# Kernel optimization log

Hardware: AMD Instinct MI355X
Metric: run time of the kernel (lower is better)

The kernel has to match this reference:

```python
import jax, jax.numpy as jnp
import numpy as np

N, IN, HID, OUT = 18432, 1024, 4096, 4096


def _quantize_per_channel(w):
    # symmetric per-output-channel int8 quantization: scale = max|w|/127
    scale = jnp.max(jnp.abs(w), axis=1) / 127.0  # [rows]
    scale = jnp.maximum(scale, 1e-8)
    w_int8 = jnp.clip(jnp.round(w / scale[:, None]), -127, 127).astype(jnp.int8)
    return w_int8, scale.astype(jnp.float32)


def setup_inputs() -> dict:
    key = jax.random.key(0)
    kx, k1, kb1, k2, kb2 = jax.random.split(key, 5)
    x = jax.random.normal(kx, (N, IN), dtype=jnp.float32)
    # kaiming-uniform-ish float weights, then per-channel int8 quantize
    bound1 = 1.0 / np.sqrt(IN)
    bound2 = 1.0 / np.sqrt(HID)
    w1 = jax.random.uniform(k1, (HID, IN), minval=-bound1, maxval=bound1, dtype=jnp.float32)
    w2 = jax.random.uniform(k2, (OUT, HID), minval=-bound2, maxval=bound2, dtype=jnp.float32)
    w1_int8, w1_scale = _quantize_per_channel(w1)
    w2_int8, w2_scale = _quantize_per_channel(w2)
    b1 = jax.random.uniform(kb1, (HID,), minval=-bound1, maxval=bound1, dtype=jnp.float32)
    b2 = jax.random.uniform(kb2, (OUT,), minval=-bound2, maxval=bound2, dtype=jnp.float32)
    return {"x": x, "w1_int8": w1_int8, "w1_scale": w1_scale, "b1": b1,
            "w2_int8": w2_int8, "w2_scale": w2_scale, "b2": b2}


def reference(x, w1_int8, w1_scale, b1, w2_int8, w2_scale, b2):
    # W8A16 dequant GEMM + fused GELU (layer 1)
    w1 = w1_int8.astype(jnp.float32) * w1_scale[:, None]  # [HID, IN]
    h = jax.nn.gelu(x @ w1.T + b1, approximate=False)      # [N, HID]
    # W8A16 dequant GEMM (layer 2)
    w2 = w2_int8.astype(jnp.float32) * w2_scale[:, None]  # [OUT, HID]
    return h @ w2.T + b2                                   # [N, OUT]
```

## Files before the change

### kernel.cpp

```cpp
#include <hip/hip_runtime.h>
#include <math.h>

#define NROWS 18432
#define IN_DIM 1024
#define HID_DIM 4096
#define OUT_DIM 4096
#define NTN 16

typedef __attribute__((ext_vector_type(8))) short bf16x8;
typedef __attribute__((ext_vector_type(4))) float f32x4;

typedef const __attribute__((address_space(1))) char gchar;
typedef __attribute__((address_space(3))) char lchar;

__device__ __forceinline__ unsigned short f2bf(float f) {
    union { float f; unsigned u; } v; v.f = f;
    unsigned r = v.u + 0x7fffu + ((v.u >> 16) & 1u);
    return (unsigned short)(r >> 16);
}

__device__ __forceinline__ f32x4 MFMA16(bf16x8 a, bf16x8 b, f32x4 c) {
    return __builtin_amdgcn_mfma_f32_16x16x32_bf16(a, b, c, 0, 0, 0);
}


__global__ void cvt_f32_bf16_k(const float4* __restrict__ in, uint4* __restrict__ out, int nvec) {
    int i = blockIdx.x * blockDim.x + threadIdx.x;
    if (i >= nvec) return;
    float4 a = in[2 * i], b = in[2 * i + 1];
    union { unsigned short s[8]; uint4 v; } o;
    o.s[0] = f2bf(a.x); o.s[1] = f2bf(a.y); o.s[2] = f2bf(a.z); o.s[3] = f2bf(a.w);
    o.s[4] = f2bf(b.x); o.s[5] = f2bf(b.y); o.s[6] = f2bf(b.z); o.s[7] = f2bf(b.w);
    out[i] = o.v;
}

__global__ void cvt_i32_bf16_k(const int4* __restrict__ in, uint4* __restrict__ out, int nvec) {
    int i = blockIdx.x * blockDim.x + threadIdx.x;
    if (i >= nvec) return;
    int4 a = in[2 * i], b = in[2 * i + 1];
    union { unsigned short s[8]; uint4 v; } o;
    o.s[0] = f2bf((float)a.x); o.s[1] = f2bf((float)a.y);
    o.s[2] = f2bf((float)a.z); o.s[3] = f2bf((float)a.w);
    o.s[4] = f2bf((float)b.x); o.s[5] = f2bf((float)b.y);
    o.s[6] = f2bf((float)b.z); o.s[7] = f2bf((float)b.w);
    out[i] = o.v;
}

template<int EPI>
__global__ __launch_bounds__(512, 2)
void gemm3b(const unsigned short* __restrict__ A, const unsigned short* __restrict__ B,
            const float* __restrict__ scale, const float* __restrict__ bias,
            void* __restrict__ Cout, int K) {
    extern __shared__ __align__(16) char sm[];

    const int tid  = threadIdx.x;
    const int lane = tid & 63;
    const int wid  = tid >> 6;
    const int wm   = wid >> 2, wn = wid & 3;

    const int nwg  = gridDim.x;
    const int q    = nwg >> 3, r = nwg & 7;
    const int xcd  = blockIdx.x & 7, bidx = blockIdx.x >> 3;
    const int swz  = xcd * q + (xcd < r ? xcd : r) + bidx;
    const int tm   = swz / NTN, tn = swz % NTN;

    const size_t rowbytes = (size_t)K * 2;
    const char* Ag = (const char*)A + (size_t)tm * 256 * rowbytes;
    const char* Bg = (const char*)B + (size_t)tn * 256 * rowbytes;

    const int l16 = lane & 15;
    const int cg  = (lane >> 4) << 4;

    f32x4  acc[8][4] = {};
    bf16x8 af[4], ah[4], bl[2], bh[2];

    const int NT = K >> 5;

#define STAGE(GB, LB, UNIT, KTB) { \
    const int po_ = ((UNIT) << 13) + (tid << 4); \
    const int r_  = po_ >> 6; \
    const int b_  = (po_ & 63) ^ (((r_ >> 1) & 3) << 4); \
    __builtin_amdgcn_global_load_lds( \
        (gchar*)((GB) + (size_t)r_ * rowbytes + (KTB) + (size_t)b_), \
        (lchar*)((LB) + po_), 16, 0, 0); \
}

#define RDA(BUF, ROW) ((BUF) + ((ROW) << 6) + (cg ^ ((((ROW) >> 1) & 3) << 4)))

#define SFENCE __builtin_amdgcn_sched_barrier(0)
#define WAITV4 { SFENCE; asm volatile("s_waitcnt vmcnt(4)"); SFENCE; }
#define WAITV0 { SFENCE; asm volatile("s_waitcnt vmcnt(0)"); SFENCE; }
#define BARR   { SFENCE; __builtin_amdgcn_s_barrier(); SFENCE; }

    {
        char* b0 = sm;
        STAGE(Ag, b0,         0, (size_t)0); STAGE(Ag, b0,         1, (size_t)0);
        STAGE(Bg, b0 + 16384, 0, (size_t)0); STAGE(Bg, b0 + 16384, 1, (size_t)0);
        char* b1 = sm + 32768;
        STAGE(Ag, b1,         0, (size_t)64); STAGE(Ag, b1,         1, (size_t)64);
        STAGE(Bg, b1 + 16384, 0, (size_t)64); STAGE(Bg, b1 + 16384, 1, (size_t)64);
    }

    for (int t = 0; t < NT; ++t) {
        if (t < NT - 1) { WAITV4; }
        else            { WAITV0; }
        BARR;

        char* Ab = sm + 32768 * (t % 3);
        char* Bb = Ab + 16384;

        const int ab = (wm << 6) + l16;
        #pragma unroll
        for (int mm = 0; mm < 4; ++mm) {
            af[mm] = *(const bf16x8*)RDA(Ab, ab + mm * 16);
            ah[mm] = *(const bf16x8*)RDA(Ab, 128 + ab + mm * 16);
        }
        const int bb = (wn << 5) + l16;
        #pragma unroll
        for (int nn = 0; nn < 2; ++nn) {
            bl[nn] = *(const bf16x8*)RDA(Bb, bb + nn * 16);
            bh[nn] = *(const bf16x8*)RDA(Bb, 128 + bb + nn * 16);
        }

        if (t + 2 < NT) {
            char* Sb = sm + 32768 * ((t + 2) % 3);
            const size_t ktb = ((size_t)(t + 2)) << 6;
            STAGE(Ag, Sb,         0, ktb); STAGE(Ag, Sb,         1, ktb);
            STAGE(Bg, Sb + 16384, 0, ktb); STAGE(Bg, Sb + 16384, 1, ktb);
        }

        #pragma unroll
        for (int mm = 0; mm < 4; ++mm)
            #pragma unroll
            for (int nn = 0; nn < 2; ++nn) {
                acc[mm][nn]         = MFMA16(af[mm], bl[nn], acc[mm][nn]);
                acc[mm][2 + nn]     = MFMA16(af[mm], bh[nn], acc[mm][2 + nn]);
                acc[4 + mm][nn]     = MFMA16(ah[mm], bl[nn], acc[4 + mm][nn]);
                acc[4 + mm][2 + nn] = MFMA16(ah[mm], bh[nn], acc[4 + mm][2 + nn]);
            }
    }
#undef STAGE
#undef RDA
#undef SFENCE
#undef WAITV4
#undef WAITV0
#undef BARR

    const int rg = (lane >> 4) << 2;
    #pragma unroll
    for (int j = 0; j < 4; ++j) {
        const int col = tn * 256 + ((j >> 1) << 7) + (wn << 5) + ((j & 1) << 4) + l16;
        const float sc = scale[col];
        const float bi = bias[col];
        #pragma unroll
        for (int m = 0; m < 8; ++m) {
            const int row0 = tm * 256 + ((m >> 2) << 7) + (wm << 6) + ((m & 3) << 4) + rg;
            #pragma unroll
            for (int rr = 0; rr < 4; ++rr) {
                float v = acc[m][j][rr] * sc + bi;
                if (EPI == 0) {
                    float g = 0.5f * v * (1.0f + erff(v * 0.70710678118654752f));
                    ((unsigned short*)Cout)[(size_t)(row0 + rr) * 4096 + col] = f2bf(g);
                } else {
                    ((float*)Cout)[(size_t)(row0 + rr) * 4096 + col] = v;
                }
            }
        }
    }
}

extern "C" void kernel_launch(void* const* d_in, const int* in_sizes, int n_in,
                              void* d_out, int out_size, void* d_ws, size_t ws_size,
                              hipStream_t stream) {
    const float* x   = (const float*)d_in[0];
    const int*   w1q = (const int*)d_in[1];
    const float* s1  = (const float*)d_in[2];
    const float* b1  = (const float*)d_in[3];
    const int*   w2q = (const int*)d_in[4];
    const float* s2  = (const float*)d_in[5];
    const float* b2  = (const float*)d_in[6];
    float*       out = (float*)d_out;

    hipFuncSetAttribute((const void*)gemm3b<0>, hipFuncAttributeMaxDynamicSharedMemorySize, 98304);
    hipFuncSetAttribute((const void*)gemm3b<1>, hipFuncAttributeMaxDynamicSharedMemorySize, 98304);

    char* ws = (char*)d_ws;
    const size_t XBF  = (size_t)NROWS   * IN_DIM  * 2;
    const size_t W1BF = (size_t)HID_DIM * IN_DIM  * 2;
    const size_t W2BF = (size_t)OUT_DIM * HID_DIM * 2;
    const size_t FIXED = XBF + W1BF + W2BF;

    unsigned short* xbf  = (unsigned short*)ws;
    unsigned short* w1bf = (unsigned short*)(ws + XBF);
    unsigned short* w2bf = (unsigned short*)(ws + XBF + W1BF);
    unsigned short* hbuf = (unsigned short*)(ws + FIXED);

    {
        int nvx = NROWS * IN_DIM / 8;
        cvt_f32_bf16_k<<<(nvx + 255) / 256, 256, 0, stream>>>((const float4*)x, (uint4*)xbf, nvx);
        int nv1 = HID_DIM * IN_DIM / 8;
        cvt_i32_bf16_k<<<(nv1 + 255) / 256, 256, 0, stream>>>((const int4*)w1q, (uint4*)w1bf, nv1);
        int nv2 = OUT_DIM * HID_DIM / 8;
        cvt_i32_bf16_k<<<(nv2 + 255) / 256, 256, 0, stream>>>((const int4*)w2q, (uint4*)w2bf, nv2);
    }

    size_t avail = (ws_size > FIXED) ? (ws_size - FIXED) : 0;
    long rp = (long)(avail / ((size_t)HID_DIM * 2));
    rp = (rp / 256) * 256;
    if (rp > NROWS) rp = NROWS;
    if (rp < 256)   rp = 256;

    for (int r0 = 0; r0 < NROWS; r0 += (int)rp) {
        int rows = (int)(((long)(NROWS - r0) < rp) ? (NROWS - r0) : rp);
        dim3 g(NTN * (rows / 256));
        gemm3b<0><<<g, 512, 98304, stream>>>(xbf + (size_t)r0 * IN_DIM, w1bf, s1, b1,
                                             (void*)hbuf, IN_DIM);
        gemm3b<1><<<g, 512, 98304, stream>>>(hbuf, w2bf, s2, b2,
                                             (void*)(out + (size_t)r0 * OUT_DIM), HID_DIM);
    }
    (void)in_sizes; (void)n_in; (void)out_size;
}
```

Before: 882.5 us.

## Split LDS fragment reads into halves interleaved with MFMA quadrants, staggered per warp row

The per-iteration LDS reads and MFMA block are split into two half-fragment loads, each followed by its own MFMA quadrant, then the cross quadrants. Warp rows 0 and 1 take the halves in opposite order so their LDS traffic and matrix work are staggered. The MFMA groups are wrapped in s_setprio raises. The aim is to overlap LDS read latency with matrix work and to cut LDS bank contention between waves, at the risk of compiler scheduling and register-pressure changes.

```diff
diff --git a/kernel.cpp b/kernel.cpp
--- a/kernel.cpp
+++ b/kernel.cpp
@@ -48,7 +48,7 @@
 
 template<int EPI>
 __global__ __launch_bounds__(512, 2)
-void gemm3b(const unsigned short* __restrict__ A, const unsigned short* __restrict__ B,
+void gemmap(const unsigned short* __restrict__ A, const unsigned short* __restrict__ B,
             const float* __restrict__ scale, const float* __restrict__ bias,
             void* __restrict__ Cout, int K) {
     extern __shared__ __align__(16) char sm[];
@@ -92,6 +92,31 @@
 #define WAITV0 { SFENCE; asm volatile("s_waitcnt vmcnt(0)"); SFENCE; }
 #define BARR   { SFENCE; __builtin_amdgcn_s_barrier(); SFENCE; }
 
+#define RH0 { _Pragma("unroll") for (int mm = 0; mm < 4; ++mm) \
+                  af[mm] = *(const bf16x8*)RDA(Ab, ab + mm * 16); \
+              _Pragma("unroll") for (int nn = 0; nn < 2; ++nn) \
+                  bl[nn] = *(const bf16x8*)RDA(Bb, bb + nn * 16); }
+#define RH1 { _Pragma("unroll") for (int mm = 0; mm < 4; ++mm) \
+                  ah[mm] = *(const bf16x8*)RDA(Ab, 128 + ab + mm * 16); \
+              _Pragma("unroll") for (int nn = 0; nn < 2; ++nn) \
+                  bh[nn] = *(const bf16x8*)RDA(Bb, 128 + bb + nn * 16); }
+#define M_A { __builtin_amdgcn_s_setprio(1); \
+              _Pragma("unroll") for (int mm = 0; mm < 4; ++mm) \
+                  _Pragma("unroll") for (int nn = 0; nn < 2; ++nn) \
+                      acc[mm][nn] = MFMA16(af[mm], bl[nn], acc[mm][nn]); \
+              __builtin_amdgcn_s_setprio(0); }
+#define M_B { __builtin_amdgcn_s_setprio(1); \
+              _Pragma("unroll") for (int mm = 0; mm < 4; ++mm) \
+                  _Pragma("unroll") for (int nn = 0; nn < 2; ++nn) \
+                      acc[4 + mm][2 + nn] = MFMA16(ah[mm], bh[nn], acc[4 + mm][2 + nn]); \
+              __builtin_amdgcn_s_setprio(0); }
+#define M_X { __builtin_amdgcn_s_setprio(1); \
+              _Pragma("unroll") for (int mm = 0; mm < 4; ++mm) \
+                  _Pragma("unroll") for (int nn = 0; nn < 2; ++nn) { \
+                      acc[mm][2 + nn] = MFMA16(af[mm], bh[nn], acc[mm][2 + nn]); \
+                      acc[4 + mm][nn] = MFMA16(ah[mm], bl[nn], acc[4 + mm][nn]); } \
+              __builtin_amdgcn_s_setprio(0); }
+
     {
         char* b0 = sm;
         STAGE(Ag, b0,         0, (size_t)0); STAGE(Ag, b0,         1, (size_t)0);
@@ -109,19 +134,6 @@
         char* Ab = sm + 32768 * (t % 3);
         char* Bb = Ab + 16384;
 
-        const int ab = (wm << 6) + l16;
-        #pragma unroll
-        for (int mm = 0; mm < 4; ++mm) {
-            af[mm] = *(const bf16x8*)RDA(Ab, ab + mm * 16);
-            ah[mm] = *(const bf16x8*)RDA(Ab, 128 + ab + mm * 16);
-        }
-        const int bb = (wn << 5) + l16;
-        #pragma unroll
-        for (int nn = 0; nn < 2; ++nn) {
-            bl[nn] = *(const bf16x8*)RDA(Bb, bb + nn * 16);
-            bh[nn] = *(const bf16x8*)RDA(Bb, 128 + bb + nn * 16);
-        }
-
         if (t + 2 < NT) {
             char* Sb = sm + 32768 * ((t + 2) % 3);
             const size_t ktb = ((size_t)(t + 2)) << 6;
@@ -129,15 +141,12 @@
             STAGE(Bg, Sb + 16384, 0, ktb); STAGE(Bg, Sb + 16384, 1, ktb);
         }
 
-        #pragma unroll
-        for (int mm = 0; mm < 4; ++mm)
-            #pragma unroll
-            for (int nn = 0; nn < 2; ++nn) {
-                acc[mm][nn]         = MFMA16(af[mm], bl[nn], acc[mm][nn]);
-                acc[mm][2 + nn]     = MFMA16(af[mm], bh[nn], acc[mm][2 + nn]);
-                acc[4 + mm][nn]     = MFMA16(ah[mm], bl[nn], acc[4 + mm][nn]);
-                acc[4 + mm][2 + nn] = MFMA16(ah[mm], bh[nn], acc[4 + mm][2 + nn]);
-            }
+        const int ab = (wm << 6) + l16;
+        const int bb = (wn << 5) + l16;
+
+        if (wm == 0) { RH0; M_A; RH1; M_B; }
+        else         { RH1; M_B; RH0; M_A; }
+        M_X;
     }
 #undef STAGE
 #undef RDA
@@ -145,6 +154,11 @@
 #undef WAITV4
 #undef WAITV0
 #undef BARR
+#undef RH0
+#undef RH1
+#undef M_A
+#undef M_B
+#undef M_X
 
     const int rg = (lane >> 4) << 2;
     #pragma unroll
@@ -181,8 +195,8 @@
     const float* b2  = (const float*)d_in[6];
     float*       out = (float*)d_out;
 
-    hipFuncSetAttribute((const void*)gemm3b<0>, hipFuncAttributeMaxDynamicSharedMemorySize, 98304);
-    hipFuncSetAttribute((const void*)gemm3b<1>, hipFuncAttributeMaxDynamicSharedMemorySize, 98304);
+    hipFuncSetAttribute((const void*)gemmap<0>, hipFuncAttributeMaxDynamicSharedMemorySize, 98304);
+    hipFuncSetAttribute((const void*)gemmap<1>, hipFuncAttributeMaxDynamicSharedMemorySize, 98304);
 
     char* ws = (char*)d_ws;
     const size_t XBF  = (size_t)NROWS   * IN_DIM  * 2;
@@ -213,9 +227,9 @@
     for (int r0 = 0; r0 < NROWS; r0 += (int)rp) {
         int rows = (int)(((long)(NROWS - r0) < rp) ? (NROWS - r0) : rp);
         dim3 g(NTN * (rows / 256));
-        gemm3b<0><<<g, 512, 98304, stream>>>(xbf + (size_t)r0 * IN_DIM, w1bf, s1, b1,
+        gemmap<0><<<g, 512, 98304, stream>>>(xbf + (size_t)r0 * IN_DIM, w1bf, s1, b1,
                                              (void*)hbuf, IN_DIM);
-        gemm3b<1><<<g, 512, 98304, stream>>>(hbuf, w2bf, s2, b2,
+        gemmap<1><<<g, 512, 98304, stream>>>(hbuf, w2bf, s2, b2,
                                              (void*)(out + (size_t)r0 * OUT_DIM), HID_DIM);
     }
     (void)in_sizes; (void)n_in; (void)out_size;
```

New measurement: 918.3 us. 4.1% more time.

## Restructure GEMM mainloop into 8-phase ping-pong schedule with K=64 tiles

Applied to the files above, without the earlier changes.

Replaces the 3-stage K=32 triple-buffered loop with a double-buffered K=64 tile scheme split into eight quadrant phases. Each phase interleaves LDS reads, staging of the next tile's half-blocks, a barrier and a block of MFMAs under raised wave priority. It also changes the LDS swizzle to 128-byte rows with an XOR over 8 columns and remaps the warp-to-output layout. LDS use rises to 128KB per block, which with launch_bounds(512,2) may limit occupancy to one block per CU, and the many extra barriers add sync cost.

```diff
diff --git a/kernel.cpp b/kernel.cpp
--- a/kernel.cpp
+++ b/kernel.cpp
@@ -48,7 +48,7 @@
 
 template<int EPI>
 __global__ __launch_bounds__(512, 2)
-void gemm3b(const unsigned short* __restrict__ A, const unsigned short* __restrict__ B,
+void gemm8q(const unsigned short* __restrict__ A, const unsigned short* __restrict__ B,
             const float* __restrict__ scale, const float* __restrict__ bias,
             void* __restrict__ Cout, int K) {
     extern __shared__ __align__(16) char sm[];
@@ -69,78 +69,91 @@
     const char* Bg = (const char*)B + (size_t)tn * 256 * rowbytes;
 
     const int l16 = lane & 15;
-    const int cg  = (lane >> 4) << 4;
+    const int cgi = lane >> 4;
+    const int sw  = l16 & 7;
+    const int c0  = ((cgi       ^ sw) << 4);
+    const int c1  = (((4 | cgi) ^ sw) << 4);
 
     f32x4  acc[8][4] = {};
-    bf16x8 af[4], ah[4], bl[2], bh[2];
-
-    const int NT = K >> 5;
-
-#define STAGE(GB, LB, UNIT, KTB) { \
-    const int po_ = ((UNIT) << 13) + (tid << 4); \
-    const int r_  = po_ >> 6; \
-    const int b_  = (po_ & 63) ^ (((r_ >> 1) & 3) << 4); \
-    __builtin_amdgcn_global_load_lds( \
-        (gchar*)((GB) + (size_t)r_ * rowbytes + (KTB) + (size_t)b_), \
-        (lchar*)((LB) + po_), 16, 0, 0); \
-}
-
-#define RDA(BUF, ROW) ((BUF) + ((ROW) << 6) + (cg ^ ((((ROW) >> 1) & 3) << 4)))
+    bf16x8 aq[4][2], bn0[2][2], bn1[2][2];
+
+    const int NIT = K >> 7;
+
+#define STAGE(GB, LDSOFF, HR, TILE) { \
+    _Pragma("unroll") for (int ld_ = 0; ld_ < 2; ++ld_) { \
+        const int po_ = (ld_ << 13) + (tid << 4); \
+        const int pr_ = po_ >> 7; \
+        const int pc_ = (po_ & 127) ^ ((pr_ & 7) << 4); \
+        __builtin_amdgcn_global_load_lds( \
+            (gchar*)((GB) + (size_t)((HR) + pr_) * rowbytes + ((size_t)(TILE) << 7) + (size_t)pc_), \
+            (lchar*)(sm + (LDSOFF) + po_), 16, 0, 0); \
+    } }
+
+#define READ_A(BUFOFF, MH) { const char* Ab_ = sm + (BUFOFF) + wm * 16384; \
+    _Pragma("unroll") for (int mm_ = 0; mm_ < 4; ++mm_) { \
+        const int ro_ = (((MH) * 64) + mm_ * 16 + l16) << 7; \
+        aq[mm_][0] = *(const bf16x8*)(Ab_ + ro_ + c0); \
+        aq[mm_][1] = *(const bf16x8*)(Ab_ + ro_ + c1); } }
+
+#define READ_B(BUFOFF, NH, DST) { const char* Bb_ = sm + (BUFOFF) + 32768 + (wn >> 1) * 16384; \
+    _Pragma("unroll") for (int nn_ = 0; nn_ < 2; ++nn_) { \
+        const int ro_ = (((wn & 1) * 64) + (NH) * 32 + nn_ * 16 + l16) << 7; \
+        DST[nn_][0] = *(const bf16x8*)(Bb_ + ro_ + c0); \
+        DST[nn_][1] = *(const bf16x8*)(Bb_ + ro_ + c1); } }
+
+#define MF(MH, NH, BQ) { __builtin_amdgcn_s_setprio(1); \
+    _Pragma("unroll") for (int mm_ = 0; mm_ < 4; ++mm_) \
+        _Pragma("unroll") for (int nn_ = 0; nn_ < 2; ++nn_) { \
+            acc[(MH)*4+mm_][(NH)*2+nn_] = MFMA16(aq[mm_][0], BQ[nn_][0], acc[(MH)*4+mm_][(NH)*2+nn_]); \
+            acc[(MH)*4+mm_][(NH)*2+nn_] = MFMA16(aq[mm_][1], BQ[nn_][1], acc[(MH)*4+mm_][(NH)*2+nn_]); } \
+    __builtin_amdgcn_s_setprio(0); }
 
 #define SFENCE __builtin_amdgcn_sched_barrier(0)
 #define WAITV4 { SFENCE; asm volatile("s_waitcnt vmcnt(4)"); SFENCE; }
 #define WAITV0 { SFENCE; asm volatile("s_waitcnt vmcnt(0)"); SFENCE; }
 #define BARR   { SFENCE; __builtin_amdgcn_s_barrier(); SFENCE; }
 
-    {
-        char* b0 = sm;
-        STAGE(Ag, b0,         0, (size_t)0); STAGE(Ag, b0,         1, (size_t)0);
-        STAGE(Bg, b0 + 16384, 0, (size_t)0); STAGE(Bg, b0 + 16384, 1, (size_t)0);
-        char* b1 = sm + 32768;
-        STAGE(Ag, b1,         0, (size_t)64); STAGE(Ag, b1,         1, (size_t)64);
-        STAGE(Bg, b1 + 16384, 0, (size_t)64); STAGE(Bg, b1 + 16384, 1, (size_t)64);
-    }
-
-    for (int t = 0; t < NT; ++t) {
-        if (t < NT - 1) { WAITV4; }
-        else            { WAITV0; }
-        BARR;
-
-        char* Ab = sm + 32768 * (t % 3);
-        char* Bb = Ab + 16384;
-
-        const int ab = (wm << 6) + l16;
-        #pragma unroll
-        for (int mm = 0; mm < 4; ++mm) {
-            af[mm] = *(const bf16x8*)RDA(Ab, ab + mm * 16);
-            ah[mm] = *(const bf16x8*)RDA(Ab, 128 + ab + mm * 16);
-        }
-        const int bb = (wn << 5) + l16;
-        #pragma unroll
-        for (int nn = 0; nn < 2; ++nn) {
-            bl[nn] = *(const bf16x8*)RDA(Bb, bb + nn * 16);
-            bh[nn] = *(const bf16x8*)RDA(Bb, 128 + bb + nn * 16);
-        }
-
-        if (t + 2 < NT) {
-            char* Sb = sm + 32768 * ((t + 2) % 3);
-            const size_t ktb = ((size_t)(t + 2)) << 6;
-            STAGE(Ag, Sb,         0, ktb); STAGE(Ag, Sb,         1, ktb);
-            STAGE(Bg, Sb + 16384, 0, ktb); STAGE(Bg, Sb + 16384, 1, ktb);
-        }
-
-        #pragma unroll
-        for (int mm = 0; mm < 4; ++mm)
-            #pragma unroll
-            for (int nn = 0; nn < 2; ++nn) {
-                acc[mm][nn]         = MFMA16(af[mm], bl[nn], acc[mm][nn]);
-                acc[mm][2 + nn]     = MFMA16(af[mm], bh[nn], acc[mm][2 + nn]);
-                acc[4 + mm][nn]     = MFMA16(ah[mm], bl[nn], acc[4 + mm][nn]);
-                acc[4 + mm][2 + nn] = MFMA16(ah[mm], bh[nn], acc[4 + mm][2 + nn]);
-            }
+    STAGE(Ag, 0,             0,   0); STAGE(Ag, 16384,         128, 0);
+    STAGE(Bg, 32768,         0,   0); STAGE(Bg, 49152,         128, 0);
+    STAGE(Bg, 65536 + 32768, 0,   1); STAGE(Bg, 65536 + 49152, 128, 1);
+    WAITV4; BARR;
+
+    const int NT = K >> 6;
+    for (int j = 0; j < NIT; ++j) {
+        const int  t0 = 2 * j, t1 = 2 * j + 1;
+        const bool p2 = (t0 + 2 < NT);
+        const bool p3 = (t1 + 2 < NT);
+        const bool lastj = (j == NIT - 1);
+
+        READ_A(0, 0); READ_B(0, 0, bn0);
+        STAGE(Ag, 65536, 0, t1);
+        BARR; MF(0, 0, bn0);
+        READ_B(0, 1, bn1);
+        STAGE(Ag, 65536 + 16384, 128, t1);
+        BARR; MF(0, 1, bn1);
+        READ_A(0, 1);
+        if (p2) STAGE(Bg, 32768, 0, t0 + 2);
+        BARR; MF(1, 1, bn1);
+        if (p2) STAGE(Bg, 49152, 128, t0 + 2);
+        if (lastj) { WAITV0; } else { WAITV4; }
+        BARR; MF(1, 0, bn0);
+        READ_A(65536, 0); READ_B(65536, 0, bn0);
+        if (p2) STAGE(Ag, 0, 0, t0 + 2);
+        BARR; MF(0, 0, bn0);
+        READ_B(65536, 1, bn1);
+        if (p2) STAGE(Ag, 16384, 128, t0 + 2);
+        BARR; MF(0, 1, bn1);
+        READ_A(65536, 1);
+        if (p3) STAGE(Bg, 65536 + 32768, 0, t1 + 2);
+        BARR; MF(1, 1, bn1);
+        if (p3) STAGE(Bg, 65536 + 49152, 128, t1 + 2);
+        if (!lastj) { WAITV4; }
+        BARR; MF(1, 0, bn0);
     }
 #undef STAGE
-#undef RDA
+#undef READ_A
+#undef READ_B
+#undef MF
 #undef SFENCE
 #undef WAITV4
 #undef WAITV0
@@ -148,16 +161,16 @@
 
     const int rg = (lane >> 4) << 2;
     #pragma unroll
-    for (int j = 0; j < 4; ++j) {
-        const int col = tn * 256 + ((j >> 1) << 7) + (wn << 5) + ((j & 1) << 4) + l16;
+    for (int nq = 0; nq < 4; ++nq) {
+        const int col = tn * 256 + wn * 64 + (nq >> 1) * 32 + (nq & 1) * 16 + l16;
         const float sc = scale[col];
         const float bi = bias[col];
         #pragma unroll
-        for (int m = 0; m < 8; ++m) {
-            const int row0 = tm * 256 + ((m >> 2) << 7) + (wm << 6) + ((m & 3) << 4) + rg;
+        for (int mq = 0; mq < 8; ++mq) {
+            const int row0 = tm * 256 + wm * 128 + (mq >> 2) * 64 + (mq & 3) * 16 + rg;
             #pragma unroll
             for (int rr = 0; rr < 4; ++rr) {
-                float v = acc[m][j][rr] * sc + bi;
+                float v = acc[mq][nq][rr] * sc + bi;
                 if (EPI == 0) {
                     float g = 0.5f * v * (1.0f + erff(v * 0.70710678118654752f));
                     ((unsigned short*)Cout)[(size_t)(row0 + rr) * 4096 + col] = f2bf(g);
@@ -181,8 +194,8 @@
     const float* b2  = (const float*)d_in[6];
     float*       out = (float*)d_out;
 
-    hipFuncSetAttribute((const void*)gemm3b<0>, hipFuncAttributeMaxDynamicSharedMemorySize, 98304);
-    hipFuncSetAttribute((const void*)gemm3b<1>, hipFuncAttributeMaxDynamicSharedMemorySize, 98304);
+    hipFuncSetAttribute((const void*)gemm8q<0>, hipFuncAttributeMaxDynamicSharedMemorySize, 131072);
+    hipFuncSetAttribute((const void*)gemm8q<1>, hipFuncAttributeMaxDynamicSharedMemorySize, 131072);
 
     char* ws = (char*)d_ws;
     const size_t XBF  = (size_t)NROWS   * IN_DIM  * 2;
@@ -213,10 +226,10 @@
     for (int r0 = 0; r0 < NROWS; r0 += (int)rp) {
         int rows = (int)(((long)(NROWS - r0) < rp) ? (NROWS - r0) : rp);
         dim3 g(NTN * (rows / 256));
-        gemm3b<0><<<g, 512, 98304, stream>>>(xbf + (size_t)r0 * IN_DIM, w1bf, s1, b1,
-                                             (void*)hbuf, IN_DIM);
-        gemm3b<1><<<g, 512, 98304, stream>>>(hbuf, w2bf, s2, b2,
-                                             (void*)(out + (size_t)r0 * OUT_DIM), HID_DIM);
+        gemm8q<0><<<g, 512, 131072, stream>>>(xbf + (size_t)r0 * IN_DIM, w1bf, s1, b1,
+                                              (void*)hbuf, IN_DIM);
+        gemm8q<1><<<g, 512, 131072, stream>>>(hbuf, w2bf, s2, b2,
+                                              (void*)(out + (size_t)r0 * OUT_DIM), HID_DIM);
     }
     (void)in_sizes; (void)n_in; (void)out_size;
 }
```

Result: faster. 826.0 us (-6.4%).

## Restructure GEMM mainloop into 4-stage LDS ring with split-phase MFMA and setprio

Applied to the files above, without the earlier changes.

Grows the LDS ring buffer from three to four 32 KB stages so each iteration can prefetch two tiles ahead without a barrier at the top of the loop. Each k-step is split into two MFMA halves: the first half's MFMAs overlap the A prefetch and the reloading of the second A fragment, and the B prefetch plus wait and barrier are placed between the halves. MFMA sections are wrapped in s_setprio, and the wave-to-tile mapping changes to contiguous 128x64 wave tiles. Dynamic LDS use rises to 128 KB per block, and the extra barrier placement could add stalls if the loads are not actually hidden.

```diff
diff --git a/kernel.cpp b/kernel.cpp
--- a/kernel.cpp
+++ b/kernel.cpp
@@ -48,7 +48,7 @@
 
 template<int EPI>
 __global__ __launch_bounds__(512, 2)
-void gemm3b(const unsigned short* __restrict__ A, const unsigned short* __restrict__ B,
+void gemm4b(const unsigned short* __restrict__ A, const unsigned short* __restrict__ B,
             const float* __restrict__ scale, const float* __restrict__ bias,
             void* __restrict__ Cout, int K) {
     extern __shared__ __align__(16) char sm[];
@@ -72,7 +72,7 @@
     const int cg  = (lane >> 4) << 4;
 
     f32x4  acc[8][4] = {};
-    bf16x8 af[4], ah[4], bl[2], bh[2];
+    bf16x8 aq[4], b0[2], b1[2];
 
     const int NT = K >> 5;
 
@@ -92,52 +92,56 @@
 #define WAITV0 { SFENCE; asm volatile("s_waitcnt vmcnt(0)"); SFENCE; }
 #define BARR   { SFENCE; __builtin_amdgcn_s_barrier(); SFENCE; }
 
-    {
-        char* b0 = sm;
-        STAGE(Ag, b0,         0, (size_t)0); STAGE(Ag, b0,         1, (size_t)0);
-        STAGE(Bg, b0 + 16384, 0, (size_t)0); STAGE(Bg, b0 + 16384, 1, (size_t)0);
-        char* b1 = sm + 32768;
-        STAGE(Ag, b1,         0, (size_t)64); STAGE(Ag, b1,         1, (size_t)64);
-        STAGE(Bg, b1 + 16384, 0, (size_t)64); STAGE(Bg, b1 + 16384, 1, (size_t)64);
-    }
+    STAGE(Ag, sm,                 0, (size_t)0); STAGE(Ag, sm,                 1, (size_t)0);
+    STAGE(Bg, sm + 16384,         0, (size_t)0); STAGE(Bg, sm + 16384,         1, (size_t)0);
+    STAGE(Ag, sm + 32768,         0, (size_t)64); STAGE(Ag, sm + 32768,         1, (size_t)64);
+    STAGE(Bg, sm + 32768 + 16384, 0, (size_t)64); STAGE(Bg, sm + 32768 + 16384, 1, (size_t)64);
+    WAITV4; BARR;
 
     for (int t = 0; t < NT; ++t) {
-        if (t < NT - 1) { WAITV4; }
-        else            { WAITV0; }
-        BARR;
-
-        char* Ab = sm + 32768 * (t % 3);
-        char* Bb = Ab + 16384;
-
-        const int ab = (wm << 6) + l16;
-        #pragma unroll
-        for (int mm = 0; mm < 4; ++mm) {
-            af[mm] = *(const bf16x8*)RDA(Ab, ab + mm * 16);
-            ah[mm] = *(const bf16x8*)RDA(Ab, 128 + ab + mm * 16);
+        const char* Ab = sm + ((t & 3) << 15);
+        const char* Bb = Ab + 16384;
+        char*       Nb = sm + (((t + 2) & 3) << 15);
+        const bool  pf  = (t + 2 < NT);
+        const size_t ktb = ((size_t)(t + 2)) << 6;
+
+        const int ar = wm * 128 + l16;
+        #pragma unroll
+        for (int mm = 0; mm < 4; ++mm) aq[mm] = *(const bf16x8*)RDA(Ab, ar + mm * 16);
+        const int br = wn * 64 + l16;
+        #pragma unroll
+        for (int nn = 0; nn < 2; ++nn) {
+            b0[nn] = *(const bf16x8*)RDA(Bb, br + nn * 16);
+            b1[nn] = *(const bf16x8*)RDA(Bb, br + 32 + nn * 16);
         }
-        const int bb = (wn << 5) + l16;
-        #pragma unroll
-        for (int nn = 0; nn < 2; ++nn) {
-            bl[nn] = *(const bf16x8*)RDA(Bb, bb + nn * 16);
-            bh[nn] = *(const bf16x8*)RDA(Bb, 128 + bb + nn * 16);
-        }
-
-        if (t + 2 < NT) {
-            char* Sb = sm + 32768 * ((t + 2) % 3);
-            const size_t ktb = ((size_t)(t + 2)) << 6;
-            STAGE(Ag, Sb,         0, ktb); STAGE(Ag, Sb,         1, ktb);
-            STAGE(Bg, Sb + 16384, 0, ktb); STAGE(Bg, Sb + 16384, 1, ktb);
-        }
-
+        if (pf) { STAGE(Ag, Nb, 0, ktb); STAGE(Ag, Nb, 1, ktb); }
+
+        __builtin_amdgcn_s_setprio(1);
         #pragma unroll
         for (int mm = 0; mm < 4; ++mm)
             #pragma unroll
             for (int nn = 0; nn < 2; ++nn) {
-                acc[mm][nn]         = MFMA16(af[mm], bl[nn], acc[mm][nn]);
-                acc[mm][2 + nn]     = MFMA16(af[mm], bh[nn], acc[mm][2 + nn]);
-                acc[4 + mm][nn]     = MFMA16(ah[mm], bl[nn], acc[4 + mm][nn]);
-                acc[4 + mm][2 + nn] = MFMA16(ah[mm], bh[nn], acc[4 + mm][2 + nn]);
+                acc[mm][nn]     = MFMA16(aq[mm], b0[nn], acc[mm][nn]);
+                acc[mm][2 + nn] = MFMA16(aq[mm], b1[nn], acc[mm][2 + nn]);
             }
+        __builtin_amdgcn_s_setprio(0);
+
+        #pragma unroll
+        for (int mm = 0; mm < 4; ++mm) aq[mm] = *(const bf16x8*)RDA(Ab, ar + 64 + mm * 16);
+        if (pf) { STAGE(Bg, Nb + 16384, 0, ktb); STAGE(Bg, Nb + 16384, 1, ktb); }
+
+        if (pf) { WAITV4; } else { WAITV0; }
+        BARR;
+
+        __builtin_amdgcn_s_setprio(1);
+        #pragma unroll
+        for (int mm = 0; mm < 4; ++mm)
+            #pragma unroll
+            for (int nn = 0; nn < 2; ++nn) {
+                acc[4 + mm][nn]     = MFMA16(aq[mm], b0[nn], acc[4 + mm][nn]);
+                acc[4 + mm][2 + nn] = MFMA16(aq[mm], b1[nn], acc[4 + mm][2 + nn]);
+            }
+        __builtin_amdgcn_s_setprio(0);
     }
 #undef STAGE
 #undef RDA
@@ -148,16 +152,16 @@
 
     const int rg = (lane >> 4) << 2;
     #pragma unroll
-    for (int j = 0; j < 4; ++j) {
-        const int col = tn * 256 + ((j >> 1) << 7) + (wn << 5) + ((j & 1) << 4) + l16;
+    for (int nq = 0; nq < 4; ++nq) {
+        const int col = tn * 256 + wn * 64 + (nq >> 1) * 32 + (nq & 1) * 16 + l16;
         const float sc = scale[col];
         const float bi = bias[col];
         #pragma unroll
-        for (int m = 0; m < 8; ++m) {
-            const int row0 = tm * 256 + ((m >> 2) << 7) + (wm << 6) + ((m & 3) << 4) + rg;
+        for (int mq = 0; mq < 8; ++mq) {
+            const int row0 = tm * 256 + wm * 128 + (mq >> 2) * 64 + (mq & 3) * 16 + rg;
             #pragma unroll
             for (int rr = 0; rr < 4; ++rr) {
-                float v = acc[m][j][rr] * sc + bi;
+                float v = acc[mq][nq][rr] * sc + bi;
                 if (EPI == 0) {
                     float g = 0.5f * v * (1.0f + erff(v * 0.70710678118654752f));
                     ((unsigned short*)Cout)[(size_t)(row0 + rr) * 4096 + col] = f2bf(g);
@@ -181,8 +185,8 @@
     const float* b2  = (const float*)d_in[6];
     float*       out = (float*)d_out;
 
-    hipFuncSetAttribute((const void*)gemm3b<0>, hipFuncAttributeMaxDynamicSharedMemorySize, 98304);
-    hipFuncSetAttribute((const void*)gemm3b<1>, hipFuncAttributeMaxDynamicSharedMemorySize, 98304);
+    hipFuncSetAttribute((const void*)gemm4b<0>, hipFuncAttributeMaxDynamicSharedMemorySize, 131072);
+    hipFuncSetAttribute((const void*)gemm4b<1>, hipFuncAttributeMaxDynamicSharedMemorySize, 131072);
 
     char* ws = (char*)d_ws;
     const size_t XBF  = (size_t)NROWS   * IN_DIM  * 2;
@@ -213,10 +217,10 @@
     for (int r0 = 0; r0 < NROWS; r0 += (int)rp) {
         int rows = (int)(((long)(NROWS - r0) < rp) ? (NROWS - r0) : rp);
         dim3 g(NTN * (rows / 256));
-        gemm3b<0><<<g, 512, 98304, stream>>>(xbf + (size_t)r0 * IN_DIM, w1bf, s1, b1,
-                                             (void*)hbuf, IN_DIM);
-        gemm3b<1><<<g, 512, 98304, stream>>>(hbuf, w2bf, s2, b2,
-                                             (void*)(out + (size_t)r0 * OUT_DIM), HID_DIM);
+        gemm4b<0><<<g, 512, 131072, stream>>>(xbf + (size_t)r0 * IN_DIM, w1bf, s1, b1,
+                                              (void*)hbuf, IN_DIM);
+        gemm4b<1><<<g, 512, 131072, stream>>>(hbuf, w2bf, s2, b2,
+                                              (void*)(out + (size_t)r0 * OUT_DIM), HID_DIM);
     }
     (void)in_sizes; (void)n_in; (void)out_size;
 }
```

New measurement: 864.3 us. 1.02x faster.
